# Kernel tuning notes

Hardware: AMD Instinct MI355X
Metric: run time of the kernel (lower is better)

Reference implementation:

```python
import jax, jax.numpy as jnp
import numpy as np

N, D = 8192, 256
SIM_THRESHOLD = 0.85
EPS = 1e-12  # matches torch F.normalize eps


def setup_inputs() -> dict:
    key = jax.random.key(0)
    k1, k2, k3 = jax.random.split(key, 3)
    return {
        "cls_embeddings": jax.random.normal(k1, (N, D), dtype=jnp.float32),
        "w1": jax.random.normal(k2, (4, 16), dtype=jnp.float32) * 0.5,
        "b1": jnp.zeros((16,), dtype=jnp.float32),
        "w2": jax.random.normal(k3, (16, 1), dtype=jnp.float32) * 0.25,
        "b2": jnp.zeros((1,), dtype=jnp.float32),
    }


def _similarity_features(cls_embeddings):
    # 4-dim features from the pairwise cosine-similarity matrix.
    n = cls_embeddings.shape[0]
    norm = jnp.maximum(jnp.linalg.norm(cls_embeddings, axis=-1, keepdims=True), EPS)
    normed = cls_embeddings / norm
    sim = normed @ normed.T                      # [n, n]
    eye = jnp.eye(n, dtype=bool)
    off = ~eye
    n_pairs = n * (n - 1)
    max_sim = jnp.where(off, sim, -jnp.inf).max()
    mean_sim = jnp.where(off, sim, 0.0).sum() / n_pairs
    frac_above = (jnp.where(off, sim, 0.0) > SIM_THRESHOLD).sum() / n_pairs

    # Connected components over edges {sim > 0.85} == union-find cluster count.
    # Min-label propagation + pointer jumping (Shiloach-Vishkin style),
    # converges in O(log n) iterations.
    adj = (jax.lax.stop_gradient(sim) > SIM_THRESHOLD) | eye  # include self
    labels0 = jnp.arange(n, dtype=jnp.int32)

    def body(_, labels):
        nb_min = jnp.where(adj, labels[None, :], n).min(axis=1).astype(jnp.int32)
        labels = jnp.minimum(labels, nb_min)
        return labels[labels]  # pointer jump

    iters = int(np.ceil(np.log2(max(n, 2)))) + 3
    labels = jax.lax.fori_loop(0, iters, body, labels0)
    cluster_count = (labels == labels0).sum() / n  # roots are component minima

    return jnp.stack([max_sim, mean_sim,
                      frac_above.astype(jnp.float32),
                      cluster_count.astype(jnp.float32)])


def reference(cls_embeddings, w1, b1, w2, b2):
    feats = _similarity_features(cls_embeddings)[None, :]          # [1, 4]
    h = jax.nn.gelu(feats @ w1 + b1, approximate=False)            # [1, 16]
    score = jax.nn.sigmoid(h @ w2 + b2)                            # [1, 1]
    return score
```

## Files before the change

kernel.cpp:

```cpp
#include <hip/hip_runtime.h>
#include <math.h>

#define NROWS 8192
#define DIM   256
#define K2    512
#define NTB   32
#define SIM_THR 0.85f

#define A2_OFF   1024
#define EDGE_OFF (1024 + NROWS * K2 * 2)

typedef _Float16 half8 __attribute__((ext_vector_type(8)));
typedef float f32x4 __attribute__((ext_vector_type(4)));

__device__ inline void load_lds16(const void* g, void* l) {
    __builtin_amdgcn_global_load_lds((const __attribute__((address_space(1))) void*)g,
                                     (__attribute__((address_space(3))) void*)l, 16, 0, 0);
}

__device__ inline void atomicMaxF(float* addr, float val) {
    if (val >= 0.f) atomicMax((int*)addr, __float_as_int(val));
    else            atomicMin((unsigned int*)addr, __float_as_uint(val));
}

__global__ __launch_bounds__(256) void prep_kernel(const float* __restrict__ x,
                                                   unsigned short* __restrict__ a2,
                                                   float* wsf) {
    if (blockIdx.x == 0 && threadIdx.x == 0) {
        wsf[0] = -INFINITY; wsf[1] = 0.f;
        ((unsigned int*)wsf)[2] = 0u; ((unsigned int*)wsf)[3] = 0u;
    }
    int row  = blockIdx.x * 4 + (threadIdx.x >> 6);
    int lane = threadIdx.x & 63;
    float4 v = ((const float4*)(x + (size_t)row * DIM))[lane];
    float ss = v.x * v.x + v.y * v.y + v.z * v.z + v.w * v.w;
    #pragma unroll
    for (int off = 32; off; off >>= 1) ss += __shfl_xor(ss, off);
    float norm = fmaxf(sqrtf(ss), 1e-12f);
    float f[4] = {v.x / norm, v.y / norm, v.z / norm, v.w / norm};
    unsigned short h[4], l[4];
    #pragma unroll
    for (int j = 0; j < 4; ++j) {
        _Float16 hh = (_Float16)f[j];
        _Float16 ll = (_Float16)(f[j] - (float)hh);
        h[j] = __builtin_bit_cast(unsigned short, hh);
        l[j] = __builtin_bit_cast(unsigned short, ll);
    }
    unsigned short* rp = a2 + (size_t)row * K2;
    *(ushort4*)(rp + lane * 4)       = make_ushort4(h[0], h[1], h[2], h[3]);
    *(ushort4*)(rp + DIM + lane * 4) = make_ushort4(l[0], l[1], l[2], l[3]);
}

__global__ __launch_bounds__(512, 2) void sim_kernel(const unsigned short* __restrict__ a2,
                                                     float* wsf, int2* edges, int cap) {
    int idx = blockIdx.x;
    int bi = (int)((sqrtf(8.f * idx + 1.f) - 1.f) * 0.5f);
    while ((bi + 1) * (bi + 2) / 2 <= idx) ++bi;
    while (bi * (bi + 1) / 2 > idx) --bi;
    int bj = idx - bi * (bi + 1) / 2;
    int i0 = bi * 256, j0 = bj * 256;

    __shared__ __align__(16) char As[2][256 * 128];
    __shared__ __align__(16) char Bs[2][256 * 128];
    __shared__ float sred[24];

    int t = threadIdx.x, lane = t & 63, w = t >> 6;
    int wr = w >> 2, wc = w & 3;

    f32x4 acc[8][4] = {};

    int perm = ((lane & 7) ^ (lane >> 3)) * 16;
    const char* gA = (const char*)a2 + (size_t)(i0 + w * 32 + (lane >> 3)) * 1024 + perm;
    const char* gB = (const char*)a2 + (size_t)(j0 + w * 32 + (lane >> 3)) * 1024 + perm;
    int ldsW = w * 32 * 128;

    int rbA = (wr * 128 + (lane & 15)) * 128;
    int rbB = (wc * 64  + (lane & 15)) * 128;
    int kx  = (lane & 7) << 4;
    int kb0 = (lane >> 4) << 4;

    #pragma unroll
    for (int q = 0; q < 4; ++q) {
        load_lds16(gA + q * 8192, As[0] + ldsW + q * 1024);
        load_lds16(gB + q * 8192, Bs[0] + ldsW + q * 1024);
    }
    __syncthreads();

    int cur = 0;
    for (int it = 0; it < 8; ++it) {
        if (it < 7) {
            int kc = (it + 1) * 128;
            #pragma unroll
            for (int q = 0; q < 4; ++q) {
                load_lds16(gA + kc + q * 8192, As[cur ^ 1] + ldsW + q * 1024);
                load_lds16(gB + kc + q * 8192, Bs[cur ^ 1] + ldsW + q * 1024);
            }
        }
        const char* A = As[cur];
        const char* B = Bs[cur];
        #pragma unroll
        for (int ks = 0; ks < 2; ++ks) {
            int kb = (ks * 64 + kb0) ^ kx;
            half8 af[8], bf[4];
            #pragma unroll
            for (int m = 0; m < 8; ++m) af[m] = *(const half8*)(A + rbA + m * 2048 + kb);
            #pragma unroll
            for (int n = 0; n < 4; ++n) bf[n] = *(const half8*)(B + rbB + n * 2048 + kb);
            #pragma unroll
            for (int m = 0; m < 8; ++m)
                #pragma unroll
                for (int n = 0; n < 4; ++n)
                    acc[m][n] = __builtin_amdgcn_mfma_f32_16x16x32_f16(af[m], bf[n], acc[m][n], 0, 0, 0);
        }
        __syncthreads();
        cur ^= 1;
    }

    bool diagT = (bi == bj);
    float        wgt  = diagT ? 1.f : 2.f;
    unsigned int wgtu = diagT ? 1u : 2u;
    float lmax = -INFINITY, lsum = 0.f;
    unsigned int lcnt = 0;
    #pragma unroll
    for (int m = 0; m < 8; ++m) {
        #pragma unroll
        for (int n = 0; n < 4; ++n) {
            #pragma unroll
            for (int j = 0; j < 4; ++j) {
                float s = acc[m][n][j];
                int gi = i0 + wr * 128 + m * 16 + (lane >> 4) * 4 + j;
                int gj = j0 + wc * 64  + n * 16 + (lane & 15);
                if (gi != gj) {
                    lmax = fmaxf(lmax, s);
                    lsum += s;
                    if (s > SIM_THR) {
                        lcnt++;
                        unsigned int e = atomicAdd(&((unsigned int*)wsf)[3], 1u);
                        if (e < (unsigned int)cap) edges[e] = make_int2(gi, gj);
                    }
                }
            }
        }
    }
    #pragma unroll
    for (int off = 32; off; off >>= 1) {
        lmax = fmaxf(lmax, __shfl_xor(lmax, off));
        lsum += __shfl_xor(lsum, off);
        lcnt += __shfl_xor(lcnt, off);
    }
    if (lane == 0) { sred[w] = lmax; sred[8 + w] = lsum; ((unsigned int*)sred)[16 + w] = lcnt; }
    __syncthreads();
    if (t == 0) {
        float bm = -INFINITY, bs = 0.f;
        unsigned int bc = 0;
        #pragma unroll
        for (int q = 0; q < 8; ++q) {
            bm = fmaxf(bm, sred[q]);
            bs += sred[8 + q];
            bc += ((unsigned int*)sred)[16 + q];
        }
        atomicMaxF(&wsf[0], bm);
        atomicAdd(&wsf[1], bs * wgt);
        if (bc) atomicAdd(&((unsigned int*)wsf)[2], bc * wgtu);
    }
}

__global__ __launch_bounds__(1024) void finalize_kernel(const float* wsf, const int2* edges, int cap,
                                                        const float* __restrict__ w1,
                                                        const float* __restrict__ b1,
                                                        const float* __restrict__ w2,
                                                        const float* __restrict__ b2,
                                                        float* __restrict__ out) {
    __shared__ int lab[NROWS];
    __shared__ int tmp[NROWS];
    __shared__ int wsum[16];
    int t = threadIdx.x;
    for (int i = t; i < NROWS; i += 1024) lab[i] = i;
    unsigned int ec = ((const unsigned int*)wsf)[3];
    if (ec > (unsigned int)cap) ec = (unsigned int)cap;
    __syncthreads();

    if (ec > 0) {
        for (int it = 0; it < 16; ++it) {
            for (int i = t; i < NROWS; i += 1024) tmp[i] = lab[i];
            __syncthreads();
            for (unsigned int e = t; e < ec; e += 1024) {
                int u = edges[e].x, v = edges[e].y;
                atomicMin(&tmp[u], lab[v]);
                atomicMin(&tmp[v], lab[u]);
            }
            __syncthreads();
            for (int i = t; i < NROWS; i += 1024) lab[i] = tmp[tmp[i]];
            __syncthreads();
        }
    }

    int lc = 0;
    for (int i = t; i < NROWS; i += 1024) lc += (lab[i] == i);
    #pragma unroll
    for (int off = 32; off; off >>= 1) lc += __shfl_xor(lc, off);
    if ((t & 63) == 0) wsum[t >> 6] = lc;
    __syncthreads();

    if (t == 0) {
        int roots = 0;
        #pragma unroll
        for (int q = 0; q < 16; ++q) roots += wsum[q];
        const float n_pairs = 67100672.0f;
        float feats[4];
        feats[0] = wsf[0];
        feats[1] = wsf[1] / n_pairs;
        feats[2] = (float)((const unsigned int*)wsf)[2] / n_pairs;
        feats[3] = (float)roots / (float)NROWS;
        float acc2 = b2[0];
        for (int j = 0; j < 16; ++j) {
            float hj = b1[j];
            #pragma unroll
            for (int i = 0; i < 4; ++i) hj = fmaf(feats[i], w1[i * 16 + j], hj);
            float g = 0.5f * hj * (1.0f + erff(hj * 0.70710678118f));
            acc2 = fmaf(g, w2[j], acc2);
        }
        out[0] = 1.0f / (1.0f + expf(-acc2));
    }
}

extern "C" void kernel_launch(void* const* d_in, const int* in_sizes, int n_in,
                              void* d_out, int out_size, void* d_ws, size_t ws_size,
                              hipStream_t stream) {
    const float* cls = (const float*)d_in[0];
    const float* w1  = (const float*)d_in[1];
    const float* b1  = (const float*)d_in[2];
    const float* w2  = (const float*)d_in[3];
    const float* b2  = (const float*)d_in[4];
    float* out = (float*)d_out;

    float* wsf = (float*)d_ws;
    unsigned short* a2 = (unsigned short*)((char*)d_ws + A2_OFF);
    int2* edges = (int2*)((char*)d_ws + EDGE_OFF);
    long long avail = (long long)ws_size - (long long)EDGE_OFF;
    int cap = (int)(avail > 0 ? (avail / 8 > 4194304 ? 4194304 : avail / 8) : 0);

    prep_kernel<<<NROWS / 4, 256, 0, stream>>>(cls, a2, wsf);
    sim_kernel<<<NTB * (NTB + 1) / 2, 512, 0, stream>>>(a2, wsf, edges, cap);
    finalize_kernel<<<1, 1024, 0, stream>>>(wsf, edges, cap, w1, b1, w2, b2, out);
}
```

Measured before the change: 138.0 us.

## Hand-schedule GEMM main loop with split barriers, waitcnt and XCD-aware block remap

The sim_kernel K-loop swaps __syncthreads for explicit s_waitcnt vmcnt plus s_barrier, so the next tile's global-to-LDS loads can stay in flight while the current tile is consumed. The MFMA work is split into four phases that load half the A fragments at a time, each wrapped in barriers and s_setprio to interleave LDS reads with matrix ops across waves. Block indices are also remapped so that consecutive triangle tiles land on the same XCD, improving L2 reuse of shared row panels. The cost is extra barriers per iteration and reliance on exact vmcnt accounting for correctness.

```diff
diff --git a/kernel.cpp b/kernel.cpp
--- a/kernel.cpp
+++ b/kernel.cpp
@@ -5,6 +5,7 @@
 #define DIM   256
 #define K2    512
 #define NTB   32
+#define NTRI  528
 #define SIM_THR 0.85f
 
 #define A2_OFF   1024
@@ -53,7 +54,8 @@
 
 __global__ __launch_bounds__(512, 2) void sim_kernel(const unsigned short* __restrict__ a2,
                                                      float* wsf, int2* edges, int cap) {
-    int idx = blockIdx.x;
+    int bid = blockIdx.x;
+    int idx = (bid & 7) * (NTRI / 8) + (bid >> 3);
     int bi = (int)((sqrtf(8.f * idx + 1.f) - 1.f) * 0.5f);
     while ((bi + 1) * (bi + 2) / 2 <= idx) ++bi;
     while (bi * (bi + 1) / 2 > idx) --bi;
@@ -84,36 +86,46 @@
         load_lds16(gA + q * 8192, As[0] + ldsW + q * 1024);
         load_lds16(gB + q * 8192, Bs[0] + ldsW + q * 1024);
     }
-    __syncthreads();
-
-    int cur = 0;
+
     for (int it = 0; it < 8; ++it) {
+        int c = it & 1;
         if (it < 7) {
             int kc = (it + 1) * 128;
             #pragma unroll
             for (int q = 0; q < 4; ++q) {
-                load_lds16(gA + kc + q * 8192, As[cur ^ 1] + ldsW + q * 1024);
-                load_lds16(gB + kc + q * 8192, Bs[cur ^ 1] + ldsW + q * 1024);
-            }
-        }
-        const char* A = As[cur];
-        const char* B = Bs[cur];
-        #pragma unroll
-        for (int ks = 0; ks < 2; ++ks) {
+                load_lds16(gA + kc + q * 8192, As[c ^ 1] + ldsW + q * 1024);
+                load_lds16(gB + kc + q * 8192, Bs[c ^ 1] + ldsW + q * 1024);
+            }
+            asm volatile("s_waitcnt vmcnt(8)" ::: "memory");
+        } else {
+            asm volatile("s_waitcnt vmcnt(0)" ::: "memory");
+        }
+        __builtin_amdgcn_s_barrier();
+
+        const char* A = As[c];
+        const char* B = Bs[c];
+        half8 bf[4];
+        #pragma unroll
+        for (int p = 0; p < 4; ++p) {
+            int ks = p >> 1, mh = p & 1;
             int kb = (ks * 64 + kb0) ^ kx;
-            half8 af[8], bf[4];
-            #pragma unroll
-            for (int m = 0; m < 8; ++m) af[m] = *(const half8*)(A + rbA + m * 2048 + kb);
-            #pragma unroll
-            for (int n = 0; n < 4; ++n) bf[n] = *(const half8*)(B + rbB + n * 2048 + kb);
-            #pragma unroll
-            for (int m = 0; m < 8; ++m)
+            if (mh == 0) {
+                #pragma unroll
+                for (int n = 0; n < 4; ++n) bf[n] = *(const half8*)(B + rbB + n * 2048 + kb);
+            }
+            half8 af[4];
+            #pragma unroll
+            for (int q = 0; q < 4; ++q) af[q] = *(const half8*)(A + rbA + (mh * 4 + q) * 2048 + kb);
+            __builtin_amdgcn_s_barrier();
+            __builtin_amdgcn_s_setprio(1);
+            #pragma unroll
+            for (int q = 0; q < 4; ++q)
                 #pragma unroll
                 for (int n = 0; n < 4; ++n)
-                    acc[m][n] = __builtin_amdgcn_mfma_f32_16x16x32_f16(af[m], bf[n], acc[m][n], 0, 0, 0);
-        }
-        __syncthreads();
-        cur ^= 1;
+                    acc[mh * 4 + q][n] = __builtin_amdgcn_mfma_f32_16x16x32_f16(af[q], bf[n], acc[mh * 4 + q][n], 0, 0, 0);
+            __builtin_amdgcn_s_setprio(0);
+            __builtin_amdgcn_s_barrier();
+        }
     }
 
     bool diagT = (bi == bj);
@@ -241,6 +253,6 @@
     int cap = (int)(avail > 0 ? (avail / 8 > 4194304 ? 4194304 : avail / 8) : 0);
 
     prep_kernel<<<NROWS / 4, 256, 0, stream>>>(cls, a2, wsf);
-    sim_kernel<<<NTB * (NTB + 1) / 2, 512, 0, stream>>>(a2, wsf, edges, cap);
+    sim_kernel<<<NTRI, 512, 0, stream>>>(a2, wsf, edges, cap);
     finalize_kernel<<<1, 1024, 0, stream>>>(wsf, edges, cap, w1, b1, w2, b2, out);
 }
```

Result: slower. 141.4 us (+2.5%).
